# Kernel tuning notes

Hardware: AMD Instinct MI355X
Metric: run time of the kernel (lower is better)

## Reference

```python
import jax, jax.numpy as jnp
import numpy as np
import math

D_MODEL = 1024
H = 16
D_K = D_MODEL // H
B = 2
S = 2048


def setup_inputs() -> dict:
    key = jax.random.key(0)
    ks = jax.random.split(key, 7)
    Q = jax.random.normal(ks[0], (B, S, D_MODEL), dtype=jnp.float32)
    K = jax.random.normal(ks[1], (B, S, D_MODEL), dtype=jnp.float32)
    V = jax.random.normal(ks[2], (B, S, D_MODEL), dtype=jnp.float32)
    # causal mask, broadcastable to [B, h, S, S]; True = keep
    mask = jnp.tril(jnp.ones((S, S), dtype=bool))[None, None, :, :]
    sc = 1.0 / math.sqrt(D_MODEL)
    W_Q = jax.random.normal(ks[3], (D_MODEL, D_MODEL), dtype=jnp.float32) * sc
    W_K = jax.random.normal(ks[4], (D_MODEL, D_MODEL), dtype=jnp.float32) * sc
    W_V = jax.random.normal(ks[5], (D_MODEL, D_MODEL), dtype=jnp.float32) * sc
    W_O = jax.random.normal(ks[6], (D_MODEL, D_MODEL), dtype=jnp.float32) * sc
    return {"Q": Q, "K": K, "V": V, "W_Q": W_Q, "W_K": W_K, "W_V": W_V, "W_O": W_O, "mask": mask}


def reference(Q, K, V, W_Q, W_K, W_V, W_O, mask):
    # Linear(d_model, d_model, bias=False): x @ W.T
    q = jnp.einsum('bsd,ed->bse', Q, W_Q).reshape(B, S, H, D_K).transpose(0, 2, 1, 3)  # [B,H,S,Dk]
    k = jnp.einsum('bsd,ed->bse', K, W_K).reshape(B, S, H, D_K).transpose(0, 2, 1, 3)
    v = jnp.einsum('bsd,ed->bse', V, W_V).reshape(B, S, H, D_K).transpose(0, 2, 1, 3)
    att = jnp.einsum('bhqd,bhkd->bhqk', q, k)  # [B,H,S,S]
    # original: masked_fill BEFORE scaling, then divide by sqrt(d_k), then softmax
    att = jnp.where(mask, att, jnp.float32(-1e15))
    att = jax.nn.softmax(att / jnp.float32(math.sqrt(D_K)), axis=3)
    out = jnp.einsum('bhqk,bhkd->bhqd', att, v)  # [B,H,S,Dk]
    out = out.transpose(0, 2, 1, 3).reshape(B, S, H * D_K)  # [B,S,d_model]
    return jnp.einsum('bsd,ed->bse', out, W_O)
```

## Files before the change

kernel.cpp:

```cpp
#include <hip/hip_runtime.h>
#include <hip/hip_bf16.h>
#include <math.h>

#define DM 1024
#define HEADS 16
#define DKH 64
#define BATCH 2
#define SEQ 2048
#define MTOK (BATCH*SEQ)
#define GK 1024
#define GN 1024

typedef __bf16 bf16;
typedef __bf16 bf16x8 __attribute__((ext_vector_type(8)));
typedef __bf16 bf16x4 __attribute__((ext_vector_type(4)));
typedef float  f32x4  __attribute__((ext_vector_type(4)));

typedef unsigned int u32_g __attribute__((address_space(1)));
typedef unsigned int u32_l __attribute__((address_space(3)));

__device__ __forceinline__ void gload_lds16(const bf16* g, bf16* lds) {
  __builtin_amdgcn_global_load_lds((const u32_g*)g, (u32_l*)lds, 16, 0, 0);
}

__device__ __forceinline__ int swze(int r) { return ((r ^ (r >> 3)) & 7) << 3; }
__device__ __forceinline__ int swzc(int r) { return (r ^ (r >> 3)) & 7; }

__global__ void cast3_k(const float* __restrict__ a, const float* __restrict__ b,
                        const float* __restrict__ c,
                        bf16* __restrict__ oa, bf16* __restrict__ ob, bf16* __restrict__ oc,
                        int n4) {
  int i = blockIdx.x * blockDim.x + threadIdx.x;
  if (i >= n4) return;
  const float* s = (blockIdx.y == 0) ? a : (blockIdx.y == 1) ? b : c;
  bf16* d = (blockIdx.y == 0) ? oa : (blockIdx.y == 1) ? ob : oc;
  float4 v = ((const float4*)s)[i];
  bf16x4 o = { (bf16)v.x, (bf16)v.y, (bf16)v.z, (bf16)v.w };
  ((bf16x4*)d)[i] = o;
}

__global__ void cast4_k(const float* __restrict__ a, const float* __restrict__ b,
                        const float* __restrict__ c, const float* __restrict__ e,
                        bf16* __restrict__ oa, bf16* __restrict__ ob,
                        bf16* __restrict__ oc, bf16* __restrict__ oe, int n4) {
  int i = blockIdx.x * blockDim.x + threadIdx.x;
  if (i >= n4) return;
  const float* s = (blockIdx.y == 0) ? a : (blockIdx.y == 1) ? b : (blockIdx.y == 2) ? c : e;
  bf16* d = (blockIdx.y == 0) ? oa : (blockIdx.y == 1) ? ob : (blockIdx.y == 2) ? oc : oe;
  float4 v = ((const float4*)s)[i];
  bf16x4 o = { (bf16)v.x, (bf16)v.y, (bf16)v.z, (bf16)v.w };
  ((bf16x4*)d)[i] = o;
}

template<typename OutT>
__device__ __forceinline__ void gemm_block(const bf16* __restrict__ A,
                                           const bf16* __restrict__ Bw,
                                           OutT* __restrict__ C) {
  __shared__ __align__(16) bf16 As[128 * 32];
  __shared__ __align__(16) bf16 Bs[128 * 32];
  const int t  = threadIdx.x;
  const int l  = t & 63;
  const int w  = t >> 6;
  const int l15 = l & 15, lg = l >> 4;
  const int brow = blockIdx.x * 128;
  const int bcol = blockIdx.y * 128;
  const int wr = (w >> 1) * 64;
  const int wc = (w & 1) * 64;
  const int lr = l >> 2;
  const int lc = (l & 3) * 8;

  f32x4 acc[4][4] = {};
  const bf16* gA = A  + (size_t)brow * GK;
  const bf16* gB = Bw + (size_t)bcol * GK;

  for (int k0 = 0; k0 < GK; k0 += 32) {
#pragma unroll
    for (int i = 0; i < 2; ++i) {
      int j = w + i * 4;
      gload_lds16(gA + (size_t)(j * 16 + lr) * GK + k0 + lc, &As[j * 512]);
      gload_lds16(gB + (size_t)(j * 16 + lr) * GK + k0 + lc, &Bs[j * 512]);
    }
    __syncthreads();
    bf16x8 af[4], bfr[4];
#pragma unroll
    for (int mf = 0; mf < 4; ++mf)
      af[mf] = *(const bf16x8*)&As[(wr + mf * 16 + l15) * 32 + lg * 8];
#pragma unroll
    for (int nf = 0; nf < 4; ++nf)
      bfr[nf] = *(const bf16x8*)&Bs[(wc + nf * 16 + l15) * 32 + lg * 8];
#pragma unroll
    for (int mf = 0; mf < 4; ++mf)
#pragma unroll
      for (int nf = 0; nf < 4; ++nf)
        acc[mf][nf] = __builtin_amdgcn_mfma_f32_16x16x32_bf16(af[mf], bfr[nf], acc[mf][nf], 0, 0, 0);
    __syncthreads();
  }
  const int crow0 = brow + wr + lg * 4;
  const int ccol0 = bcol + wc + l15;
#pragma unroll
  for (int mf = 0; mf < 4; ++mf)
#pragma unroll
    for (int nf = 0; nf < 4; ++nf)
#pragma unroll
      for (int j = 0; j < 4; ++j)
        C[(size_t)(crow0 + mf * 16 + j) * GN + (ccol0 + nf * 16)] = (OutT)acc[mf][nf][j];
}

__global__ __launch_bounds__(256) void proj_gemm(
    const bf16* __restrict__ Qb, const bf16* __restrict__ Kb, const bf16* __restrict__ Vb,
    const bf16* __restrict__ Wq, const bf16* __restrict__ Wk, const bf16* __restrict__ Wv,
    bf16* __restrict__ qp, bf16* __restrict__ kp, bf16* __restrict__ vp) {
  const bf16* A; const bf16* Bw; bf16* C;
  if (blockIdx.z == 0)      { A = Qb; Bw = Wq; C = qp; }
  else if (blockIdx.z == 1) { A = Kb; Bw = Wk; C = kp; }
  else                      { A = Vb; Bw = Wv; C = vp; }
  gemm_block<bf16>(A, Bw, C);
}

__global__ __launch_bounds__(256) void out_gemm(const bf16* __restrict__ ctx,
                                                const bf16* __restrict__ Wo,
                                                float* __restrict__ out) {
  gemm_block<float>(ctx, Wo, out);
}


__device__ __forceinline__ void vt_pack_store(bf16* __restrict__ VTb, uint4 v,
                                              int srow, int schk) {
  uint4 p;
  p.x = (unsigned)__shfl_xor((int)v.x, 8);
  p.y = (unsigned)__shfl_xor((int)v.y, 8);
  p.z = (unsigned)__shfl_xor((int)v.z, 8);
  p.w = (unsigned)__shfl_xor((int)v.w, 8);
  const int dk0 = schk * 8;
  const int cp = srow & ~1;
  if ((srow & 1) == 0) {
    unsigned w0 = (v.x & 0xffffu) | (p.x << 16);
    unsigned w1 = (v.x >> 16)     | (p.x & 0xffff0000u);
    unsigned w2 = (v.y & 0xffffu) | (p.y << 16);
    unsigned w3 = (v.y >> 16)     | (p.y & 0xffff0000u);
    *(unsigned*)&VTb[(dk0 + 0) * 64 + (cp ^ swze(dk0 + 0))] = w0;
    *(unsigned*)&VTb[(dk0 + 1) * 64 + (cp ^ swze(dk0 + 1))] = w1;
    *(unsigned*)&VTb[(dk0 + 2) * 64 + (cp ^ swze(dk0 + 2))] = w2;
    *(unsigned*)&VTb[(dk0 + 3) * 64 + (cp ^ swze(dk0 + 3))] = w3;
  } else {
    unsigned w0 = (p.z & 0xffffu) | (v.z << 16);
    unsigned w1 = (p.z >> 16)     | (v.z & 0xffff0000u);
    unsigned w2 = (p.w & 0xffffu) | (v.w << 16);
    unsigned w3 = (p.w >> 16)     | (v.w & 0xffff0000u);
    *(unsigned*)&VTb[(dk0 + 4) * 64 + (cp ^ swze(dk0 + 4))] = w0;
    *(unsigned*)&VTb[(dk0 + 5) * 64 + (cp ^ swze(dk0 + 5))] = w1;
    *(unsigned*)&VTb[(dk0 + 6) * 64 + (cp ^ swze(dk0 + 6))] = w2;
    *(unsigned*)&VTb[(dk0 + 7) * 64 + (cp ^ swze(dk0 + 7))] = w3;
  }
}

__global__ __launch_bounds__(512) void attn_k(const bf16* __restrict__ qp,
                                              const bf16* __restrict__ kp,
                                              const bf16* __restrict__ vp,
                                              bf16* __restrict__ ctx) {
  __shared__ __align__(16) bf16 Ks[2][64 * 64];
  __shared__ __align__(16) bf16 VT[2][64 * 64];
  __shared__ __align__(16) bf16 Ps[128 * 64];
  const int t = threadIdx.x;
  const int l = t & 63;
  const int w = t >> 6;
  const int l15 = l & 15, lg = l >> 4;
  const int qt = (SEQ / 128 - 1) - blockIdx.x;
  const int bh = blockIdx.y;
  const int b  = bh >> 4;
  const int h  = bh & 15;
  const int q0 = qt * 128;
  const size_t base = (size_t)(b * SEQ) * DM + h * DKH;

  const int srow = t >> 3;
  const int schk = t & 7;
  const int kSrcOff = (schk ^ swzc(srow)) * 8;

  bf16x8 qf[2];
#pragma unroll
  for (int kk = 0; kk < 2; ++kk)
    qf[kk] = *(const bf16x8*)&qp[base + (size_t)(q0 + w * 16 + l15) * DM + kk * 32 + lg * 8];

  f32x4 acc_o[4] = {};
  float lsum[4] = {0.f, 0.f, 0.f, 0.f};

  const int nkt = 2 * qt + 2;

  {
    gload_lds16(kp + base + (size_t)srow * DM + kSrcOff, &Ks[0][w * 512]);
    uint4 v0 = *(const uint4*)&vp[base + (size_t)srow * DM + schk * 8];
    vt_pack_store(VT[0], v0, srow, schk);
  }
  __syncthreads();

  for (int kt = 0; kt < nkt; ++kt) {
    const int cur = kt & 1;
    const bf16* Kc = Ks[cur];
    const bf16* Vc = VT[cur];
    const bool hasnext = (kt + 1) < nkt;
    uint4 vnx;
    if (hasnext) {
      const size_t rb = base + (size_t)((kt + 1) * 64 + srow) * DM;
      gload_lds16(kp + rb + kSrcOff, &Ks[cur ^ 1][w * 512]);
      vnx = *(const uint4*)&vp[rb + schk * 8];
    }

    f32x4 av[4];
    __builtin_amdgcn_s_setprio(1);
#pragma unroll
    for (int nf = 0; nf < 4; ++nf) {
      f32x4 a = {0.f, 0.f, 0.f, 0.f};
      const int key = nf * 16 + l15;
#pragma unroll
      for (int kk = 0; kk < 2; ++kk) {
        bf16x8 kf = *(const bf16x8*)&Kc[key * 64 + ((kk * 32 + lg * 8) ^ swze(key))];
        a = __builtin_amdgcn_mfma_f32_16x16x32_bf16(qf[kk], kf, a, 0, 0, 0);
      }
      av[nf] = a;
    }
    __builtin_amdgcn_s_setprio(0);

    float p[4][4];
    if (kt >= 2 * qt) {
#pragma unroll
      for (int nf = 0; nf < 4; ++nf) {
        const int keyg = kt * 64 + nf * 16 + l15;
#pragma unroll
        for (int j = 0; j < 4; ++j) {
          const int qg = q0 + w * 16 + lg * 4 + j;
          p[nf][j] = (keyg <= qg) ? __expf(av[nf][j] * 0.125f) : 0.f;
        }
      }
    } else {
#pragma unroll
      for (int nf = 0; nf < 4; ++nf)
#pragma unroll
        for (int j = 0; j < 4; ++j)
          p[nf][j] = __expf(av[nf][j] * 0.125f);
    }
#pragma unroll
    for (int j = 0; j < 4; ++j)
#pragma unroll
      for (int nf = 0; nf < 4; ++nf)
        lsum[j] += p[nf][j];

#pragma unroll
    for (int nf = 0; nf < 4; ++nf)
#pragma unroll
      for (int j = 0; j < 4; ++j) {
        const int row = w * 16 + lg * 4 + j;
        Ps[row * 64 + ((nf * 16 + l15) ^ swze(row))] = (bf16)p[nf][j];
      }

    const int prow = w * 16 + l15;
    __builtin_amdgcn_s_setprio(1);
#pragma unroll
    for (int kk2 = 0; kk2 < 2; ++kk2) {
      bf16x8 pf = *(const bf16x8*)&Ps[prow * 64 + ((kk2 * 32 + lg * 8) ^ swze(prow))];
#pragma unroll
      for (int nf2 = 0; nf2 < 4; ++nf2) {
        const int dk = nf2 * 16 + l15;
        bf16x8 vf = *(const bf16x8*)&Vc[dk * 64 + ((kk2 * 32 + lg * 8) ^ swze(dk))];
        acc_o[nf2] = __builtin_amdgcn_mfma_f32_16x16x32_bf16(pf, vf, acc_o[nf2], 0, 0, 0);
      }
    }
    __builtin_amdgcn_s_setprio(0);

    if (hasnext) vt_pack_store(VT[cur ^ 1], vnx, srow, schk);
    __syncthreads();
  }

  float rden[4];
#pragma unroll
  for (int j = 0; j < 4; ++j) {
    float Ls = lsum[j];
#pragma unroll
    for (int d = 1; d < 16; d <<= 1) Ls += __shfl_xor(Ls, d);
    rden[j] = 1.0f / Ls;
  }

#pragma unroll
  for (int nf2 = 0; nf2 < 4; ++nf2)
#pragma unroll
    for (int j = 0; j < 4; ++j) {
      const int qrow = q0 + w * 16 + lg * 4 + j;
      const int dk = nf2 * 16 + l15;
      ctx[base + (size_t)qrow * DM + dk] = (bf16)(acc_o[nf2][j] * rden[j]);
    }
}

extern "C" void kernel_launch(void* const* d_in, const int* in_sizes, int n_in,
                              void* d_out, int out_size, void* d_ws, size_t ws_size,
                              hipStream_t stream) {
  const float* Q  = (const float*)d_in[0];
  const float* K  = (const float*)d_in[1];
  const float* V  = (const float*)d_in[2];
  const float* WQ = (const float*)d_in[3];
  const float* WK = (const float*)d_in[4];
  const float* WV = (const float*)d_in[5];
  const float* WO = (const float*)d_in[6];

  char* ws = (char*)d_ws;
  const size_t MB = 1024 * 1024;
  bf16* Qb    = (bf16*)(ws + 0 * MB);
  bf16* Kb    = (bf16*)(ws + 8 * MB);
  bf16* Vb    = (bf16*)(ws + 16 * MB);
  bf16* Wqb   = (bf16*)(ws + 24 * MB);
  bf16* Wkb   = (bf16*)(ws + 26 * MB);
  bf16* Wvb   = (bf16*)(ws + 28 * MB);
  bf16* Wob   = (bf16*)(ws + 30 * MB);
  bf16* qproj = (bf16*)(ws + 32 * MB);
  bf16* kproj = (bf16*)(ws + 40 * MB);
  bf16* vproj = (bf16*)(ws + 48 * MB);
  bf16* ctx   = (bf16*)(ws + 56 * MB);

  const int n4t = MTOK * DM / 4;
  const int n4w = DM * DM / 4;
  dim3 gc3((n4t + 255) / 256, 3);
  cast3_k<<<gc3, 256, 0, stream>>>(Q, K, V, Qb, Kb, Vb, n4t);
  dim3 gc4((n4w + 255) / 256, 4);
  cast4_k<<<gc4, 256, 0, stream>>>(WQ, WK, WV, WO, Wqb, Wkb, Wvb, Wob, n4w);

  dim3 gProj(MTOK / 128, GN / 128, 3);
  proj_gemm<<<gProj, 256, 0, stream>>>(Qb, Kb, Vb, Wqb, Wkb, Wvb, qproj, kproj, vproj);

  dim3 gAttn(SEQ / 128, BATCH * HEADS);
  attn_k<<<gAttn, 512, 0, stream>>>(qproj, kproj, vproj, ctx);

  dim3 gOut(MTOK / 128, GN / 128, 1);
  out_gemm<<<gOut, 256, 0, stream>>>(ctx, Wob, (float*)d_out);
}
```

Baseline: 253.0 us.

## Reorder causal attention tile schedule and pack P stores via DPP lane swap

```diff
diff --git a/kernel.cpp b/kernel.cpp
--- a/kernel.cpp
+++ b/kernel.cpp
@@ -25,6 +25,18 @@
 
 __device__ __forceinline__ int swze(int r) { return ((r ^ (r >> 3)) & 7) << 3; }
 __device__ __forceinline__ int swzc(int r) { return (r ^ (r >> 3)) & 7; }
+
+__device__ __forceinline__ float dpp_swap1(float x) {
+  int i = __builtin_bit_cast(int, x);
+  i = __builtin_amdgcn_mov_dpp(i, 0xB1, 0xF, 0xF, true);
+  return __builtin_bit_cast(float, i);
+}
+
+__device__ __forceinline__ unsigned pk_bf16(float lo, float hi) {
+  unsigned a = (unsigned)__builtin_bit_cast(unsigned short, (bf16)lo);
+  unsigned b = (unsigned)__builtin_bit_cast(unsigned short, (bf16)hi);
+  return a | (b << 16);
+}
 
 __global__ void cast3_k(const float* __restrict__ a, const float* __restrict__ b,
                         const float* __restrict__ c,
@@ -165,8 +177,10 @@
   const int l = t & 63;
   const int w = t >> 6;
   const int l15 = l & 15, lg = l >> 4;
-  const int qt = (SEQ / 128 - 1) - blockIdx.x;
-  const int bh = blockIdx.y;
+  const int L  = blockIdx.x;
+  const int bh = L & 31;
+  const int m  = L >> 5;
+  const int qt = (m < 8) ? (15 - m) : (m - 8);
   const int b  = bh >> 4;
   const int h  = bh & 15;
   const int q0 = qt * 128;
@@ -244,13 +258,25 @@
       for (int nf = 0; nf < 4; ++nf)
         lsum[j] += p[nf][j];
 
-#pragma unroll
-    for (int nf = 0; nf < 4; ++nf)
+    {
+      const int par = l15 & 1;
+      const int c2  = l15 & ~1;
 #pragma unroll
       for (int j = 0; j < 4; ++j) {
         const int row = w * 16 + lg * 4 + j;
-        Ps[row * 64 + ((nf * 16 + l15) ^ swze(row))] = (bf16)p[nf][j];
+        const int rs  = swze(row);
+        float r0 = dpp_swap1(p[0][j]);
+        float r1 = dpp_swap1(p[1][j]);
+        float r2 = dpp_swap1(p[2][j]);
+        float r3 = dpp_swap1(p[3][j]);
+        unsigned dwA = par ? pk_bf16(r2, p[2][j]) : pk_bf16(p[0][j], r0);
+        unsigned dwB = par ? pk_bf16(r3, p[3][j]) : pk_bf16(p[1][j], r1);
+        const int nfA = par ? 2 : 0;
+        const int nfB = par ? 3 : 1;
+        *(unsigned*)&Ps[row * 64 + ((nfA * 16 + c2) ^ rs)] = dwA;
+        *(unsigned*)&Ps[row * 64 + ((nfB * 16 + c2) ^ rs)] = dwB;
       }
+    }
 
     const int prow = w * 16 + l15;
     __builtin_amdgcn_s_setprio(1);
@@ -324,8 +350,7 @@
   dim3 gProj(MTOK / 128, GN / 128, 3);
   proj_gemm<<<gProj, 256, 0, stream>>>(Qb, Kb, Vb, Wqb, Wkb, Wvb, qproj, kproj, vproj);
 
-  dim3 gAttn(SEQ / 128, BATCH * HEADS);
-  attn_k<<<gAttn, 512, 0, stream>>>(qproj, kproj, vproj, ctx);
+  attn_k<<<dim3(512), 512, 0, stream>>>(qproj, kproj, vproj, ctx);
 
   dim3 gOut(MTOK / 128, GN / 128, 1);
   out_gemm<<<gOut, 256, 0, stream>>>(ctx, Wob, (float*)d_out);
```

After: 229.6 us. -9.2%, faster.
